# Performance work log

Measured on AMD Instinct MI355X. Metric: run time of the kernel, lower is better.

The kernel has to match this reference:

```python
import jax, jax.numpy as jnp
import numpy as np

DELTA = 10.0
EPS = 1e-08
THRESHOLD = 0.9
STEEPNESS = 10.0


def setup_inputs() -> dict:
    key = jax.random.key(0)
    k1, k2 = jax.random.split(key)
    B, T2, T1, F = 16, 2048, 512, 128
    mels = jax.random.normal(k1, (B, T2, F), dtype=jnp.float32)
    alpha = jax.random.uniform(k2, (B, T2, T1), dtype=jnp.float32)
    mel_mask = jnp.ones((B, T2), dtype=jnp.int32)
    text_mask = jnp.ones((B, T1), dtype=jnp.int32)
    return {"mels": mels, "alpha": alpha, "mel_mask": mel_mask, "text_mask": text_mask}


def reference(mels, alpha, mel_mask, text_mask):
    B, T2, F = mels.shape
    T1 = text_mask.shape[-1]
    audio_mask = mel_mask.astype(bool)
    txt_mask = text_mask.astype(bool)
    am_f = audio_mask.astype(alpha.dtype)  # [B, T2]
    tm_f = txt_mask.astype(alpha.dtype)    # [B, T1]

    # index vector p: [B, T1]
    p = jnp.broadcast_to(jnp.arange(T1, dtype=alpha.dtype), (B, T1))

    # cosine similarity between consecutive frames (F.normalize: x / max(||x||, 1e-12))
    norm = jnp.maximum(jnp.linalg.norm(mels, axis=-1, keepdims=True), 1e-12)
    z_norm = mels / norm
    cosine_sim = jnp.sum(z_norm[:, :-1] * z_norm[:, 1:], axis=-1)  # [B, T2-1]
    activity = jax.nn.sigmoid(STEEPNESS * (THRESHOLD - cosine_sim))
    activity = jnp.concatenate([jnp.ones((B, 1), dtype=activity.dtype), activity], axis=-1)
    activity = activity * am_f

    # soft monotonic index via gated cumsum of alpha-proposal increments
    imv_proposal = jnp.einsum('bts,bs->bt', alpha, p)  # [B, T2]
    delta_prop = jnp.concatenate(
        [jnp.zeros((B, 1), dtype=imv_proposal.dtype), jnp.diff(imv_proposal, axis=-1)], axis=-1)
    eff_delta = jnp.clip(delta_prop * activity, 0.0, 1.0)
    imv = jnp.cumsum(eff_delta, axis=-1) * am_f

    # rescale so last valid frame maps to last phoneme index
    last_idx = jnp.maximum(audio_mask.sum(-1).astype(jnp.int32) - 1, 0)  # [B]
    last_val = jnp.maximum(jnp.take_along_axis(imv, last_idx[:, None], axis=1)[:, 0], 1e-06)
    text_len = txt_mask.sum(-1).astype(imv.dtype)
    scale = jnp.maximum(text_len - 1.0, 0.0) / last_val
    imv = imv * scale[:, None] * am_f

    # gamma: masked softmax over phonemes of -delta * (imv - p)^2
    dist_sq = (imv[:, :, None] - p[:, None, :]) ** 2  # [B, T2, T1]
    logits = jnp.where(txt_mask[:, None, :], -DELTA * dist_sq, -1e9)
    gamma = jax.nn.softmax(logits, axis=-1) * am_f[:, :, None]

    # durations: soft mass per phoneme
    durations = jnp.sum(gamma * am_f[:, :, None], axis=1) * tm_f  # [B, T1]

    # attention-pooling of mel frames onto phonemes
    w = jnp.swapaxes(gamma, 1, 2) * am_f[:, None, :]  # [B, T1, T2]
    w = w / (jnp.sum(w, axis=-1, keepdims=True) + EPS)
    aligned_mels = jnp.einsum('bst,btf->bsf', w, mels) * tm_f[:, :, None]  # [B, T1, F]
    return aligned_mels, durations, imv
```

## Files before the change

kernel.cpp:

```cpp
#include <hip/hip_runtime.h>
#include <math.h>
#include <cstddef>

#define B_  16
#define T2_ 2048
#define T1_ 512
#define F_  128

constexpr float DELTA_C  = 10.0f;
constexpr float EPS_C    = 1e-8f;
constexpr float THRESH_C = 0.9f;
constexpr float STEEP_C  = 10.0f;

typedef float f4v __attribute__((ext_vector_type(4)));

__global__ __launch_bounds__(256) void actprop_kernel(const float* __restrict__ mels,
                                                      const float* __restrict__ alpha,
                                                      const int* __restrict__ mel_mask,
                                                      float* __restrict__ act,
                                                      float* __restrict__ prop) {
    int wv   = (int)((blockIdx.x * blockDim.x + threadIdx.x) >> 6);
    int lane = threadIdx.x & 63;
    int il   = lane & 15;
    int r    = wv * 4 + (lane >> 4);
    int t    = r & (T2_ - 1);

    const f4v* arow = (const f4v*)(alpha + (size_t)r * T1_);
    f4v a0 = __builtin_nontemporal_load(&arow[il]);
    f4v a1 = __builtin_nontemporal_load(&arow[il + 16]);
    f4v a2 = __builtin_nontemporal_load(&arow[il + 32]);
    f4v a3 = __builtin_nontemporal_load(&arow[il + 48]);
    f4v a4 = __builtin_nontemporal_load(&arow[il + 64]);
    f4v a5 = __builtin_nontemporal_load(&arow[il + 80]);
    f4v a6 = __builtin_nontemporal_load(&arow[il + 96]);
    f4v a7 = __builtin_nontemporal_load(&arow[il + 112]);

    int rm = (t == 0) ? r : (r - 1);
    const f4v* my = (const f4v*)(mels + (size_t)r  * F_);
    const f4v* mx = (const f4v*)(mels + (size_t)rm * F_);
    f4v y0 = my[il * 2], y1 = my[il * 2 + 1];
    f4v x0 = mx[il * 2], x1 = mx[il * 2 + 1];

    float d  = x0.x*y0.x + x0.y*y0.y + x0.z*y0.z + x0.w*y0.w
             + x1.x*y1.x + x1.y*y1.y + x1.z*y1.z + x1.w*y1.w;
    float n0 = x0.x*x0.x + x0.y*x0.y + x0.z*x0.z + x0.w*x0.w
             + x1.x*x1.x + x1.y*x1.y + x1.z*x1.z + x1.w*x1.w;
    float n1 = y0.x*y0.x + y0.y*y0.y + y0.z*y0.z + y0.w*y0.w
             + y1.x*y1.x + y1.y*y1.y + y1.z*y1.z + y1.w*y1.w;

    float fb = (float)(il * 4);
    float psum;
    psum  = a0.x*(fb      ) + a0.y*(fb +   1.f) + a0.z*(fb +   2.f) + a0.w*(fb +   3.f);
    psum += a1.x*(fb+ 64.f) + a1.y*(fb +  65.f) + a1.z*(fb +  66.f) + a1.w*(fb +  67.f);
    psum += a2.x*(fb+128.f) + a2.y*(fb + 129.f) + a2.z*(fb + 130.f) + a2.w*(fb + 131.f);
    psum += a3.x*(fb+192.f) + a3.y*(fb + 193.f) + a3.z*(fb + 194.f) + a3.w*(fb + 195.f);
    psum += a4.x*(fb+256.f) + a4.y*(fb + 257.f) + a4.z*(fb + 258.f) + a4.w*(fb + 259.f);
    psum += a5.x*(fb+320.f) + a5.y*(fb + 321.f) + a5.z*(fb + 322.f) + a5.w*(fb + 323.f);
    psum += a6.x*(fb+384.f) + a6.y*(fb + 385.f) + a6.z*(fb + 386.f) + a6.w*(fb + 387.f);
    psum += a7.x*(fb+448.f) + a7.y*(fb + 449.f) + a7.z*(fb + 450.f) + a7.w*(fb + 451.f);

    for (int off = 8; off > 0; off >>= 1) {
        psum += __shfl_xor(psum, off, 64);
        d    += __shfl_xor(d,    off, 64);
        n0   += __shfl_xor(n0,   off, 64);
        n1   += __shfl_xor(n1,   off, 64);
    }

    if (il == 0) {
        float a_val;
        if (t == 0) {
            a_val = 1.0f;
        } else {
            float cs = d / (fmaxf(sqrtf(n0), 1e-12f) * fmaxf(sqrtf(n1), 1e-12f));
            a_val = 1.0f / (1.0f + __expf(-STEEP_C * (THRESH_C - cs)));
        }
        act[r]  = a_val * (float)mel_mask[r];
        prop[r] = psum;
    }
}

__global__ __launch_bounds__(512) void scan_kernel(const float* __restrict__ prop,
                                                   const float* __restrict__ act,
                                                   const int* __restrict__ mel_mask,
                                                   const int* __restrict__ text_mask,
                                                   float* __restrict__ imv_out,
                                                   float2* __restrict__ packed,
                                                   int2* __restrict__ bounds) {
    int b    = blockIdx.x;
    int tid  = threadIdx.x;
    int wave = tid >> 6, lane = tid & 63;
    __shared__ float s_imv[T2_];
    __shared__ float s_wsum[8];
    __shared__ int   s_am8[8], s_tm8[8];
    __shared__ int   s_tm[T1_];

    const float* pr = prop + (size_t)b * T2_;
    const float* ac = act  + (size_t)b * T2_;
    const int*   mm = mel_mask  + (size_t)b * T2_;
    const int*   tm = text_mask + (size_t)b * T1_;

    int tmv = tm[tid];
    s_tm[tid] = tmv;

    int t0 = tid * 4;
    f4v  pv = *(const f4v*)(pr + t0);
    f4v  av = *(const f4v*)(ac + t0);
    int4 mv = *(const int4*)(mm + t0);
    float prm1 = (tid == 0) ? 0.0f : pr[t0 - 1];

    float d0 = (tid == 0) ? 0.0f : (pv.x - prm1) * av.x;
    float d1 = (pv.y - pv.x) * av.y;
    float d2 = (pv.z - pv.y) * av.z;
    float d3 = (pv.w - pv.z) * av.w;
    d0 = fminf(fmaxf(d0, 0.0f), 1.0f);
    d1 = fminf(fmaxf(d1, 0.0f), 1.0f);
    d2 = fminf(fmaxf(d2, 0.0f), 1.0f);
    d3 = fminf(fmaxf(d3, 0.0f), 1.0f);

    float e[4];
    int   mmv[4];
    e[0] = d0; e[1] = e[0] + d1; e[2] = e[1] + d2; e[3] = e[2] + d3;
    mmv[0] = mv.x; mmv[1] = mv.y; mmv[2] = mv.z; mmv[3] = mv.w;
    float run = e[3];
    int am_local = mv.x + mv.y + mv.z + mv.w;

    int tm_local = tmv;
    for (int off = 32; off > 0; off >>= 1) {
        am_local += __shfl_xor(am_local, off, 64);
        tm_local += __shfl_xor(tm_local, off, 64);
    }
    if (lane == 0) { s_am8[wave] = am_local; s_tm8[wave] = tm_local; }

    float v = run;
    for (int off = 1; off < 64; off <<= 1) {
        float u = __shfl_up(v, off, 64);
        if (lane >= off) v += u;
    }
    if (lane == 63) s_wsum[wave] = v;
    __syncthreads();

    float woff = 0.0f;
    for (int w = 0; w < 8; w++) woff += (w < wave) ? s_wsum[w] : 0.0f;
    float excl = woff + v - run;
    {
        f4v sv = { (e[0] + excl) * (float)mmv[0],
                   (e[1] + excl) * (float)mmv[1],
                   (e[2] + excl) * (float)mmv[2],
                   (e[3] + excl) * (float)mmv[3] };
        *(f4v*)(s_imv + t0) = sv;
    }
    __syncthreads();

    int am_total = 0, tm_total = 0;
    for (int w = 0; w < 8; w++) { am_total += s_am8[w]; tm_total += s_tm8[w]; }
    int last_idx = max(am_total - 1, 0);
    float last_val = fmaxf(s_imv[last_idx], 1e-6f);
    float scale = fmaxf((float)tm_total - 1.0f, 0.0f) / last_val;
    __syncthreads();

    f4v vvv, keyv, rv;
    #pragma unroll
    for (int i = 0; i < 4; i++) {
        int t = t0 + i;
        int valid = mmv[i];
        float vv = s_imv[t] * scale * (float)valid;
        vvv[i] = vv;
        int c = (int)floorf(vv);
        float Z = 0.0f;
        for (int s = c - 2; s <= c + 3; s++) {
            if (s >= 0 && s < T1_ && s_tm[s]) {
                float dd = vv - (float)s;
                Z += __expf(-DELTA_C * dd * dd);
            }
        }
        Z = fmaxf(Z, 1e-30f);
        keyv[i] = valid ? vv : 3.0e4f;
        rv[i]   = valid ? (1.0f / Z) : 0.0f;
    }
    *(f4v*)(imv_out + (size_t)b * T2_ + t0) = vvv;
    {
        f4v p01 = { keyv[0], rv[0], keyv[1], rv[1] };
        f4v p23 = { keyv[2], rv[2], keyv[3], rv[3] };
        f4v* pko = (f4v*)(packed + (size_t)b * T2_ + t0);
        pko[0] = p01;
        pko[1] = p23;
        f4v* sk = (f4v*)(s_imv + t0);
        *sk = keyv;
    }
    __syncthreads();

    {
        int s = tid;
        float lov = (float)s - 3.0f, hiv = (float)s + 3.0f;
        int lo = 0, hi = T2_;
        while (lo < hi) { int mid = (lo + hi) >> 1; if (s_imv[mid] >= lov) hi = mid; else lo = mid + 1; }
        int st = lo;
        hi = T2_;
        while (lo < hi) { int mid = (lo + hi) >> 1; if (s_imv[mid] > hiv) hi = mid; else lo = mid + 1; }
        int2 be = {st, lo};
        bounds[(size_t)b * T1_ + s] = be;
    }
}

__global__ __launch_bounds__(256) void pool_kernel(const float* __restrict__ mels,
                                                   const int* __restrict__ text_mask,
                                                   const float2* __restrict__ packed,
                                                   const int2* __restrict__ bounds,
                                                   float* __restrict__ aligned,
                                                   float* __restrict__ dur) {
    int wid  = (int)((blockIdx.x * blockDim.x + threadIdx.x) >> 6);
    int lane = threadIdx.x & 63;
    if (wid >= B_ * (T1_ / 2)) return;
    int b = wid >> 8, s0 = (wid & 255) * 2;
    int half = lane >> 5, hl = lane & 31;
    float fs0 = (float)s0, fs1 = fs0 + 1.0f;

    const float2* pk   = packed + (size_t)b * T2_;
    const f4v*    mel4 = (const f4v*)(mels + (size_t)b * T2_ * F_);
    int2 b0 = bounds[(size_t)b * T1_ + s0];
    int2 b1 = bounds[(size_t)b * T1_ + s0 + 1];
    int t_lo = b0.x, t_hi = b1.y;

    float ax0 = 0.f, ay0 = 0.f, az0 = 0.f, aw0 = 0.f, g0s = 0.f;
    float ax1 = 0.f, ay1 = 0.f, az1 = 0.f, aw1 = 0.f, g1s = 0.f;
    for (int t = t_lo; t < t_hi; t += 2) {
        int  tl = t + half;
        bool on = tl < t_hi;
        int  ts = on ? tl : t;
        float2 p = pk[ts];
        f4v    m = mel4[(size_t)ts * 32 + hl];
        float d0 = p.x - fs0, d1 = p.x - fs1;
        float g0 = on ? __expf(-DELTA_C * d0 * d0) * p.y : 0.0f;
        float g1 = on ? __expf(-DELTA_C * d1 * d1) * p.y : 0.0f;
        g0s += g0; g1s += g1;
        ax0 += g0 * m.x; ay0 += g0 * m.y; az0 += g0 * m.z; aw0 += g0 * m.w;
        ax1 += g1 * m.x; ay1 += g1 * m.y; az1 += g1 * m.z; aw1 += g1 * m.w;
    }

    g0s += __shfl_xor(g0s, 32, 64);
    g1s += __shfl_xor(g1s, 32, 64);
    ax0 += __shfl_xor(ax0, 32, 64);
    ay0 += __shfl_xor(ay0, 32, 64);
    az0 += __shfl_xor(az0, 32, 64);
    aw0 += __shfl_xor(aw0, 32, 64);
    ax1 += __shfl_xor(ax1, 32, 64);
    ay1 += __shfl_xor(ay1, 32, 64);
    az1 += __shfl_xor(az1, 32, 64);
    aw1 += __shfl_xor(aw1, 32, 64);

    float tm0 = (float)text_mask[(size_t)b * T1_ + s0];
    float tm1 = (float)text_mask[(size_t)b * T1_ + s0 + 1];
    float inv0 = tm0 / (g0s + EPS_C);
    float inv1 = tm1 / (g1s + EPS_C);

    f4v out;
    if (half == 0) {
        out.x = ax0 * inv0; out.y = ay0 * inv0; out.z = az0 * inv0; out.w = aw0 * inv0;
    } else {
        out.x = ax1 * inv1; out.y = ay1 * inv1; out.z = az1 * inv1; out.w = aw1 * inv1;
    }
    float* obase = aligned + ((size_t)b * T1_ + s0 + half) * F_;
    ((f4v*)obase)[hl] = out;
    if (lane == 0)  dur[(size_t)b * T1_ + s0]     = g0s * tm0;
    if (lane == 32) dur[(size_t)b * T1_ + s0 + 1] = g1s * tm1;
}

extern "C" void kernel_launch(void* const* d_in, const int* in_sizes, int n_in,
                              void* d_out, int out_size, void* d_ws, size_t ws_size,
                              hipStream_t stream) {
    const float* mels      = (const float*)d_in[0];
    const float* alpha     = (const float*)d_in[1];
    const int*   mel_mask  = (const int*)d_in[2];
    const int*   text_mask = (const int*)d_in[3];

    float* out     = (float*)d_out;
    float* aligned = out;
    float* dur     = out + (size_t)B_ * T1_ * F_;
    float* imv     = dur + (size_t)B_ * T1_;

    float*  ws     = (float*)d_ws;
    float*  act    = ws;
    float*  prop   = ws + (size_t)B_ * T2_;
    float2* packed = (float2*)(ws + 2 * (size_t)B_ * T2_);
    int2*   bounds = (int2*)(ws + 4 * (size_t)B_ * T2_);

    actprop_kernel<<<(B_ * T2_) / 16, dim3(256), 0, stream>>>(mels, alpha, mel_mask, act, prop);
    scan_kernel   <<<B_,              dim3(512), 0, stream>>>(prop, act, mel_mask, text_mask, imv, packed, bounds);
    pool_kernel   <<<(B_ * T1_ / 2) / 4, dim3(256), 0, stream>>>(mels, text_mask, packed, bounds, aligned, dur);
}
```

Before: 128.1 us.

## Replace per-phoneme binary search with scatter bounds and pool four phonemes per wave

The per-phoneme binary searches over sorted imv keys in the scan kernel are replaced by a scatter: each frame writes its index into the start and end arrays for the phoneme range its key interval covers. The pool kernel now handles four phonemes per wave instead of two, so each mel row and packed value it loads is reused across twice as many outputs and half as many waves are launched. The cost is more accumulator registers, which may lower occupancy, and longer per-wave loops over a wider frame window.

```diff
diff --git a/kernel.cpp b/kernel.cpp
--- a/kernel.cpp
+++ b/kernel.cpp
@@ -85,7 +85,8 @@
                                                    const int* __restrict__ text_mask,
                                                    float* __restrict__ imv_out,
                                                    float2* __restrict__ packed,
-                                                   int2* __restrict__ bounds) {
+                                                   int* __restrict__ bstart,
+                                                   int* __restrict__ bend) {
     int b    = blockIdx.x;
     int tid  = threadIdx.x;
     int wave = tid >> 6, lane = tid & 63;
@@ -190,79 +191,105 @@
     __syncthreads();
 
     {
-        int s = tid;
-        float lov = (float)s - 3.0f, hiv = (float)s + 3.0f;
-        int lo = 0, hi = T2_;
-        while (lo < hi) { int mid = (lo + hi) >> 1; if (s_imv[mid] >= lov) hi = mid; else lo = mid + 1; }
-        int st = lo;
-        hi = T2_;
-        while (lo < hi) { int mid = (lo + hi) >> 1; if (s_imv[mid] > hiv) hi = mid; else lo = mid + 1; }
-        int2 be = {st, lo};
-        bounds[(size_t)b * T1_ + s] = be;
+        int* bs = bstart + (size_t)b * T1_;
+        int* be = bend   + (size_t)b * T1_;
+        float kprev = (tid == 0) ? -100.0f : s_imv[t0 - 1];
+        #pragma unroll
+        for (int i = 0; i < 4; i++) {
+            float k0 = fmaxf((i == 0) ? kprev : keyv[i - 1], -100.0f);
+            float k1 = keyv[i];
+            int t = t0 + i;
+            int slo = (int)floorf(k0 + 3.0f) + 1; if (slo < 0) slo = 0;
+            int shi = (int)floorf(k1 + 3.0f);     if (shi > T1_ - 1) shi = T1_ - 1;
+            for (int s = slo; s <= shi; s++) bs[s] = t;
+            slo = (int)ceilf(k0 - 3.0f);          if (slo < 0) slo = 0;
+            shi = (int)ceilf(k1 - 3.0f) - 1;      if (shi > T1_ - 1) shi = T1_ - 1;
+            for (int s = slo; s <= shi; s++) be[s] = t;
+        }
+        if (tid == 511) {
+            float k0 = fmaxf(keyv[3], -100.0f);
+            int slo = (int)floorf(k0 + 3.0f) + 1; if (slo < 0) slo = 0;
+            for (int s = slo; s <= T1_ - 1; s++) bs[s] = T2_;
+            slo = (int)ceilf(k0 - 3.0f);          if (slo < 0) slo = 0;
+            for (int s = slo; s <= T1_ - 1; s++) be[s] = T2_;
+        }
     }
 }
 
 __global__ __launch_bounds__(256) void pool_kernel(const float* __restrict__ mels,
                                                    const int* __restrict__ text_mask,
                                                    const float2* __restrict__ packed,
-                                                   const int2* __restrict__ bounds,
+                                                   const int* __restrict__ bstart,
+                                                   const int* __restrict__ bend,
                                                    float* __restrict__ aligned,
                                                    float* __restrict__ dur) {
     int wid  = (int)((blockIdx.x * blockDim.x + threadIdx.x) >> 6);
     int lane = threadIdx.x & 63;
-    if (wid >= B_ * (T1_ / 2)) return;
-    int b = wid >> 8, s0 = (wid & 255) * 2;
+    if (wid >= B_ * (T1_ / 4)) return;
+    int b = wid >> 7, s0 = (wid & 127) * 4;
     int half = lane >> 5, hl = lane & 31;
-    float fs0 = (float)s0, fs1 = fs0 + 1.0f;
+    float fs0 = (float)s0, fs1 = fs0 + 1.0f, fs2 = fs0 + 2.0f, fs3 = fs0 + 3.0f;
 
     const float2* pk   = packed + (size_t)b * T2_;
     const f4v*    mel4 = (const f4v*)(mels + (size_t)b * T2_ * F_);
-    int2 b0 = bounds[(size_t)b * T1_ + s0];
-    int2 b1 = bounds[(size_t)b * T1_ + s0 + 1];
-    int t_lo = b0.x, t_hi = b1.y;
+    int t_lo = bstart[(size_t)b * T1_ + s0];
+    int t_hi = bend  [(size_t)b * T1_ + s0 + 3];
 
     float ax0 = 0.f, ay0 = 0.f, az0 = 0.f, aw0 = 0.f, g0s = 0.f;
     float ax1 = 0.f, ay1 = 0.f, az1 = 0.f, aw1 = 0.f, g1s = 0.f;
+    float ax2 = 0.f, ay2 = 0.f, az2 = 0.f, aw2 = 0.f, g2s = 0.f;
+    float ax3 = 0.f, ay3 = 0.f, az3 = 0.f, aw3 = 0.f, g3s = 0.f;
     for (int t = t_lo; t < t_hi; t += 2) {
         int  tl = t + half;
         bool on = tl < t_hi;
         int  ts = on ? tl : t;
         float2 p = pk[ts];
         f4v    m = mel4[(size_t)ts * 32 + hl];
-        float d0 = p.x - fs0, d1 = p.x - fs1;
-        float g0 = on ? __expf(-DELTA_C * d0 * d0) * p.y : 0.0f;
-        float g1 = on ? __expf(-DELTA_C * d1 * d1) * p.y : 0.0f;
-        g0s += g0; g1s += g1;
+        float e0 = p.x - fs0, e1 = p.x - fs1, e2 = p.x - fs2, e3 = p.x - fs3;
+        float g0 = on ? __expf(-DELTA_C * e0 * e0) * p.y : 0.0f;
+        float g1 = on ? __expf(-DELTA_C * e1 * e1) * p.y : 0.0f;
+        float g2 = on ? __expf(-DELTA_C * e2 * e2) * p.y : 0.0f;
+        float g3 = on ? __expf(-DELTA_C * e3 * e3) * p.y : 0.0f;
+        g0s += g0; g1s += g1; g2s += g2; g3s += g3;
         ax0 += g0 * m.x; ay0 += g0 * m.y; az0 += g0 * m.z; aw0 += g0 * m.w;
         ax1 += g1 * m.x; ay1 += g1 * m.y; az1 += g1 * m.z; aw1 += g1 * m.w;
-    }
-
-    g0s += __shfl_xor(g0s, 32, 64);
-    g1s += __shfl_xor(g1s, 32, 64);
-    ax0 += __shfl_xor(ax0, 32, 64);
-    ay0 += __shfl_xor(ay0, 32, 64);
-    az0 += __shfl_xor(az0, 32, 64);
-    aw0 += __shfl_xor(aw0, 32, 64);
-    ax1 += __shfl_xor(ax1, 32, 64);
-    ay1 += __shfl_xor(ay1, 32, 64);
-    az1 += __shfl_xor(az1, 32, 64);
-    aw1 += __shfl_xor(aw1, 32, 64);
-
-    float tm0 = (float)text_mask[(size_t)b * T1_ + s0];
-    float tm1 = (float)text_mask[(size_t)b * T1_ + s0 + 1];
+        ax2 += g2 * m.x; ay2 += g2 * m.y; az2 += g2 * m.z; aw2 += g2 * m.w;
+        ax3 += g3 * m.x; ay3 += g3 * m.y; az3 += g3 * m.z; aw3 += g3 * m.w;
+    }
+
+    g0s += __shfl_xor(g0s, 32, 64);  g1s += __shfl_xor(g1s, 32, 64);
+    g2s += __shfl_xor(g2s, 32, 64);  g3s += __shfl_xor(g3s, 32, 64);
+    ax0 += __shfl_xor(ax0, 32, 64);  ay0 += __shfl_xor(ay0, 32, 64);
+    az0 += __shfl_xor(az0, 32, 64);  aw0 += __shfl_xor(aw0, 32, 64);
+    ax1 += __shfl_xor(ax1, 32, 64);  ay1 += __shfl_xor(ay1, 32, 64);
+    az1 += __shfl_xor(az1, 32, 64);  aw1 += __shfl_xor(aw1, 32, 64);
+    ax2 += __shfl_xor(ax2, 32, 64);  ay2 += __shfl_xor(ay2, 32, 64);
+    az2 += __shfl_xor(az2, 32, 64);  aw2 += __shfl_xor(aw2, 32, 64);
+    ax3 += __shfl_xor(ax3, 32, 64);  ay3 += __shfl_xor(ay3, 32, 64);
+    az3 += __shfl_xor(az3, 32, 64);  aw3 += __shfl_xor(aw3, 32, 64);
+
+    int4 tmq = *(const int4*)(text_mask + (size_t)b * T1_ + s0);
+    float tm0 = (float)tmq.x, tm1 = (float)tmq.y, tm2 = (float)tmq.z, tm3 = (float)tmq.w;
     float inv0 = tm0 / (g0s + EPS_C);
     float inv1 = tm1 / (g1s + EPS_C);
-
-    f4v out;
+    float inv2 = tm2 / (g2s + EPS_C);
+    float inv3 = tm3 / (g3s + EPS_C);
+
+    f4v oA, oB;
     if (half == 0) {
-        out.x = ax0 * inv0; out.y = ay0 * inv0; out.z = az0 * inv0; out.w = aw0 * inv0;
+        oA.x = ax0 * inv0; oA.y = ay0 * inv0; oA.z = az0 * inv0; oA.w = aw0 * inv0;
+        oB.x = ax1 * inv1; oB.y = ay1 * inv1; oB.z = az1 * inv1; oB.w = aw1 * inv1;
     } else {
-        out.x = ax1 * inv1; out.y = ay1 * inv1; out.z = az1 * inv1; out.w = aw1 * inv1;
-    }
-    float* obase = aligned + ((size_t)b * T1_ + s0 + half) * F_;
-    ((f4v*)obase)[hl] = out;
-    if (lane == 0)  dur[(size_t)b * T1_ + s0]     = g0s * tm0;
-    if (lane == 32) dur[(size_t)b * T1_ + s0 + 1] = g1s * tm1;
+        oA.x = ax2 * inv2; oA.y = ay2 * inv2; oA.z = az2 * inv2; oA.w = aw2 * inv2;
+        oB.x = ax3 * inv3; oB.y = ay3 * inv3; oB.z = az3 * inv3; oB.w = aw3 * inv3;
+    }
+    float* base = aligned + ((size_t)b * T1_ + s0 + 2 * half) * F_;
+    ((f4v*)base)[hl] = oA;
+    ((f4v*)(base + F_))[hl] = oB;
+    if (lane == 0) {
+        f4v dv = { g0s * tm0, g1s * tm1, g2s * tm2, g3s * tm3 };
+        *(f4v*)(dur + (size_t)b * T1_ + s0) = dv;
+    }
 }
 
 extern "C" void kernel_launch(void* const* d_in, const int* in_sizes, int n_in,
@@ -282,9 +309,10 @@
     float*  act    = ws;
     float*  prop   = ws + (size_t)B_ * T2_;
     float2* packed = (float2*)(ws + 2 * (size_t)B_ * T2_);
-    int2*   bounds = (int2*)(ws + 4 * (size_t)B_ * T2_);
+    int*    bstart = (int*)(ws + 4 * (size_t)B_ * T2_);
+    int*    bend   = bstart + (size_t)B_ * T1_;
 
     actprop_kernel<<<(B_ * T2_) / 16, dim3(256), 0, stream>>>(mels, alpha, mel_mask, act, prop);
-    scan_kernel   <<<B_,              dim3(512), 0, stream>>>(prop, act, mel_mask, text_mask, imv, packed, bounds);
-    pool_kernel   <<<(B_ * T1_ / 2) / 4, dim3(256), 0, stream>>>(mels, text_mask, packed, bounds, aligned, dur);
+    scan_kernel   <<<B_,              dim3(512), 0, stream>>>(prop, act, mel_mask, text_mask, imv, packed, bstart, bend);
+    pool_kernel   <<<(B_ * (T1_ / 4)) / 4, dim3(256), 0, stream>>>(mels, text_mask, packed, bstart, bend, aligned, dur);
 }
```

New measurement: 128.1 us. About the same (-0.0%).
